# Performance work log

Hardware: AMD Instinct MI355X
Metric: run time of the kernel (lower is better)

## Reference

```python
import jax, jax.numpy as jnp
import numpy as np

HIDDEN = 4096
INTER = 11008
BATCH, SEQ = 2, 2048


def setup_inputs() -> dict:
    key = jax.random.key(0)
    ks = jax.random.split(key, 7)
    s_h = 1.0 / np.sqrt(HIDDEN)   # nn.Linear default init bound fan_in=HIDDEN
    s_i = 1.0 / np.sqrt(INTER)    # fan_in=INTER for down_proj
    return {
        "hidden_states": jax.random.normal(ks[0], (BATCH, SEQ, HIDDEN), dtype=jnp.float32),
        "w_gate": jax.random.uniform(ks[1], (INTER, HIDDEN), jnp.float32, -s_h, s_h),
        "b_gate": jax.random.uniform(ks[2], (INTER,), jnp.float32, -s_h, s_h),
        "w_up": jax.random.uniform(ks[3], (INTER, HIDDEN), jnp.float32, -s_h, s_h),
        "b_up": jax.random.uniform(ks[4], (INTER,), jnp.float32, -s_h, s_h),
        "w_down": jax.random.uniform(ks[5], (HIDDEN, INTER), jnp.float32, -s_i, s_i),
        "b_down": jax.random.uniform(ks[6], (HIDDEN,), jnp.float32, -s_i, s_i),
    }


def reference(hidden_states, w_gate, b_gate, w_up, b_up, w_down, b_down):
    # SwiGLU MLP: down( silu(gate(x)) * up(x) )
    gate = jax.nn.silu(jnp.einsum("bsh,ih->bsi", hidden_states, w_gate) + b_gate)
    up = jnp.einsum("bsh,ih->bsi", hidden_states, w_up) + b_up
    return jnp.einsum("bsi,hi->bsh", gate * up, w_down) + b_down
```

## Files before the change

### kernel.cpp

```cpp
#include <hip/hip_runtime.h>
#include <hip/hip_bf16.h>


#define M_TOK 4096
#define HID   4096
#define INT_  11008

typedef __attribute__((ext_vector_type(8))) short bf16x8;
typedef __attribute__((ext_vector_type(4))) float f32x4;

__device__ __forceinline__ unsigned short f2bf(float f) {
    union { float f; unsigned int u; } a; a.f = f;
    unsigned int u = a.u;
    u += 0x7fff + ((u >> 16) & 1);
    return (unsigned short)(u >> 16);
}

__device__ __forceinline__ float bf2f(unsigned short h) {
    union { unsigned int u; float f; } a; a.u = ((unsigned int)h) << 16;
    return a.f;
}

__global__ void cvt_f32_bf16(const float* __restrict__ in, unsigned short* __restrict__ out, int n4) {
    int stride = gridDim.x * blockDim.x;
    for (int i = blockIdx.x * blockDim.x + threadIdx.x; i < n4; i += stride) {
        float4 v = ((const float4*)in)[i];
        ushort4 o;
        o.x = f2bf(v.x); o.y = f2bf(v.y); o.z = f2bf(v.z); o.w = f2bf(v.w);
        ((ushort4*)out)[i] = o;
    }
}

#define GLL(gsrc, ldst) \
    __builtin_amdgcn_global_load_lds( \
        (__attribute__((address_space(1))) void*)(gsrc), \
        (__attribute__((address_space(3))) void*)(ldst), 16, 0, 0)

template<int EPI>
__global__ __launch_bounds__(512, 2)
void gemm256(const unsigned short* __restrict__ A,
             const unsigned short* __restrict__ B,
             const float* __restrict__ bias,
             const unsigned short* __restrict__ gbuf,
             void* __restrict__ Cv,
             int M, int N, int K) {
    __shared__ unsigned short lds[2 * 32768];

    const int tid  = threadIdx.x;
    const int lane = tid & 63;
    const int w    = tid >> 6;
    const int wm   = w >> 2;
    const int wn   = w & 3;

    const int ntn = N >> 8;
    const int chunk = gridDim.x >> 3;
    const int sw = (blockIdx.x & 7) * chunk + (blockIdx.x >> 3);
    const int bm = sw / ntn, bn = sw % ntn;

    const unsigned short* Ag = A + (size_t)(bm * 256) * K;
    const unsigned short* Bg = B + (size_t)(bn * 256) * K;

    int offA[2][2], offB[2][2];
#pragma unroll
    for (int h = 0; h < 2; ++h)
#pragma unroll
        for (int i = 0; i < 2; ++i) {
            int sig = i * 512 + tid;
            int r   = sig >> 3;
            int s   = (sig & 7) ^ (r & 7);
            int grow = ((r >> 6) * 2 + h) * 64 + (r & 63);
            int gcol = ((r >> 5) * 2 + h) * 32 + (r & 31);
            offA[h][i] = grow * K + s * 8;
            offB[h][i] = gcol * K + s * 8;
        }

    const int rl = lane & 15;
    const int kg = lane >> 4;
    const int x  = rl & 7;
    const int aRow = (wm * 64 + rl) * 64;
    const int bRow = 16384 + (wn * 32 + rl) * 64;
    int slt[2];
#pragma unroll
    for (int ks = 0; ks < 2; ++ks) slt[ks] = ((ks * 4 + kg) ^ x) * 8;

    f32x4 acc[2][2][8];
#pragma unroll
    for (int qm = 0; qm < 2; ++qm)
#pragma unroll
        for (int qn = 0; qn < 2; ++qn)
#pragma unroll
            for (int f = 0; f < 8; ++f)
                acc[qm][qn][f] = (f32x4){0.f, 0.f, 0.f, 0.f};

    const int NT = K >> 6;

#define STAGE_A(H, DST, SRC) \
    GLL((SRC) + offA[H][0], (DST) + (H) * 8192 + tid * 8); \
    GLL((SRC) + offA[H][1], (DST) + (H) * 8192 + 4096 + tid * 8)
#define STAGE_B(H, DST, SRC) \
    GLL((SRC) + offB[H][0], (DST) + 16384 + (H) * 8192 + tid * 8); \
    GLL((SRC) + offB[H][1], (DST) + 16384 + (H) * 8192 + 4096 + tid * 8)

#define RD_A(BUF, QM, DST) \
    { _Pragma("unroll") for (int ks = 0; ks < 2; ++ks) \
      _Pragma("unroll") for (int fm = 0; fm < 4; ++fm) \
        DST[ks * 4 + fm] = *(const bf16x8*)((BUF) + (QM) * 8192 + aRow + fm * 1024 + slt[ks]); }
#define RD_B(BUF, QN, DST) \
    { _Pragma("unroll") for (int ks = 0; ks < 2; ++ks) \
      _Pragma("unroll") for (int fn = 0; fn < 2; ++fn) \
        DST[ks * 2 + fn] = *(const bf16x8*)((BUF) + (QN) * 8192 + bRow + fn * 1024 + slt[ks]); }
#define Q16(QM, QN, AF, BF) \
    { _Pragma("unroll") for (int ks = 0; ks < 2; ++ks) \
      _Pragma("unroll") for (int fm = 0; fm < 4; ++fm) \
      _Pragma("unroll") for (int fn = 0; fn < 2; ++fn) \
        acc[QM][QN][fm * 2 + fn] = __builtin_amdgcn_mfma_f32_16x16x32_bf16( \
            AF[ks * 4 + fm], BF[ks * 2 + fn], acc[QM][QN][fm * 2 + fn], 0, 0, 0); }
#define VMC(n) asm volatile("s_waitcnt vmcnt(" #n ")" ::: "memory")
#define BARR __builtin_amdgcn_s_barrier()
#define PIN  __builtin_amdgcn_sched_barrier(0)

    bf16x8 A0f[8], A1f[8], B0f[4], B1f[4];

    STAGE_A(0, lds, Ag); STAGE_B(0, lds, Bg); STAGE_B(1, lds, Bg); STAGE_A(1, lds, Ag);
    VMC(2);
    BARR; PIN;

    for (int t = 0; t < NT; ++t) {
        const unsigned short* bc = lds + (t & 1) * 32768;
        unsigned short* sb = lds + ((t + 1) & 1) * 32768;
        const int ts = (t + 1 < NT) ? (t + 1) : (NT - 1);
        const unsigned short* sAt = Ag + (size_t)ts * 64;
        const unsigned short* sBt = Bg + (size_t)ts * 64;

        RD_A(bc, 0, A0f);
        RD_B(bc, 0, B0f);
        STAGE_A(0, sb, sAt);
        Q16(0, 0, A0f, B0f);
        RD_B(bc, 1, B1f);
        STAGE_B(0, sb, sBt);
        Q16(0, 1, A0f, B1f);
        STAGE_B(1, sb, sBt);
        VMC(6);
        BARR; PIN;

        RD_A(bc, 1, A1f);
        STAGE_A(1, sb, sAt);
        Q16(1, 1, A1f, B1f);
        Q16(1, 0, A1f, B0f);
        VMC(2);
        BARR; PIN;
    }
#undef RD_A
#undef RD_B
#undef Q16
#undef VMC
#undef BARR
#undef PIN
#undef STAGE_A
#undef STAGE_B

    const int rbase = bm * 256 + wm * 128 + (lane >> 4) * 4;
    const int cbase = bn * 256 + wn * 64 + (lane & 15);
#pragma unroll
    for (int qm = 0; qm < 2; ++qm)
#pragma unroll
        for (int qn = 0; qn < 2; ++qn)
#pragma unroll
            for (int fn = 0; fn < 2; ++fn) {
                const int col = cbase + qn * 32 + fn * 16;
                const float bv = bias[col];
#pragma unroll
                for (int fm = 0; fm < 4; ++fm) {
                    const int rb = rbase + qm * 64 + fm * 16;
#pragma unroll
                    for (int j = 0; j < 4; ++j) {
                        const size_t idx = (size_t)(rb + j) * (size_t)N + col;
                        float v = acc[qm][qn][fm * 2 + fn][j] + bv;
                        if (EPI == 0) {
                            ((unsigned short*)Cv)[idx] = f2bf(v);
                        } else if (EPI == 1) {
                            float g = bf2f(gbuf[idx]);
                            float s = g / (1.f + __expf(-g));
                            ((unsigned short*)Cv)[idx] = f2bf(s * v);
                        } else {
                            ((float*)Cv)[idx] = v;
                        }
                    }
                }
            }
}

extern "C" void kernel_launch(void* const* d_in, const int* in_sizes, int n_in,
                              void* d_out, int out_size, void* d_ws, size_t ws_size,
                              hipStream_t stream) {
    const float* x  = (const float*)d_in[0];
    const float* wg = (const float*)d_in[1];
    const float* bg = (const float*)d_in[2];
    const float* wu = (const float*)d_in[3];
    const float* bu = (const float*)d_in[4];
    const float* wd = (const float*)d_in[5];
    const float* bd = (const float*)d_in[6];

    const size_t NX = (size_t)M_TOK * HID;
    const size_t NW = (size_t)INT_ * HID;

    unsigned short* ws = (unsigned short*)d_ws;
    unsigned short* Xb = ws;
    unsigned short* S1 = Xb + NX;
    unsigned short* S2 = S1 + NW;
    unsigned short* S3 = S2 + NW;

    dim3 blk512(512);
    dim3 blk256(256);
    const int CG = 2048;

    cvt_f32_bf16<<<CG, blk256, 0, stream>>>(x,  Xb, (int)(NX / 4));
    cvt_f32_bf16<<<CG, blk256, 0, stream>>>(wg, S1, (int)(NW / 4));
    gemm256<0><<<dim3(16 * 43), blk512, 0, stream>>>(Xb, S1, bg, (const unsigned short*)nullptr,
                                                     (void*)S2, M_TOK, INT_, HID);
    cvt_f32_bf16<<<CG, blk256, 0, stream>>>(wu, S3, (int)(NW / 4));
    gemm256<1><<<dim3(16 * 43), blk512, 0, stream>>>(Xb, S3, bu, S2,
                                                     (void*)S1, M_TOK, INT_, HID);
    cvt_f32_bf16<<<CG, blk256, 0, stream>>>(wd, S2, (int)(NW / 4));
    gemm256<2><<<dim3(16 * 16), blk512, 0, stream>>>(S1, S2, bd, (const unsigned short*)nullptr,
                                                     d_out, M_TOK, HID, INT_);
}
```

Measured before the change: 1.079 ms.

## Fuse gate and up projections into one dual-weight GEMM with SwiGLU epilogue

Replaces the separate gate and up GEMMs with a single kernel that computes 256x128 tiles of both projections, sharing each staged A tile between the two weight matrices. The SiLU-times-up product is applied in the epilogue, so the intermediate gate tensor is never written to and re-read from memory. The grid doubles to cover the narrower N tiles. In exchange, each A tile is now loaded once per 128 columns instead of once per 256, and the tile shape changes.

Measured after the change: 1.013 ms. 1.06x faster.

```diff
diff --git a/kernel.cpp b/kernel.cpp
--- a/kernel.cpp
+++ b/kernel.cpp
@@ -36,13 +36,161 @@
         (__attribute__((address_space(1))) void*)(gsrc), \
         (__attribute__((address_space(3))) void*)(ldst), 16, 0, 0)
 
-template<int EPI>
+#define VMC(n) asm volatile("s_waitcnt vmcnt(" #n ")" ::: "memory")
+#define BARR __builtin_amdgcn_s_barrier()
+#define PIN  __builtin_amdgcn_sched_barrier(0)
+
 __global__ __launch_bounds__(512, 2)
-void gemm256(const unsigned short* __restrict__ A,
+void gemm_gu(const unsigned short* __restrict__ A,
+             const unsigned short* __restrict__ Wg,
+             const unsigned short* __restrict__ Wu,
+             const float* __restrict__ bg,
+             const float* __restrict__ bu,
+             unsigned short* __restrict__ T,
+             int M, int NI, int K) {
+    __shared__ unsigned short lds[2 * 32768];
+
+    const int tid  = threadIdx.x;
+    const int lane = tid & 63;
+    const int w    = tid >> 6;
+    const int wm   = w >> 2;
+    const int wn   = w & 3;
+
+    const int ntn = NI >> 7;
+    const int chunk = gridDim.x >> 3;
+    const int sw = (blockIdx.x & 7) * chunk + (blockIdx.x >> 3);
+    const int bm = sw / ntn, bn = sw % ntn;
+
+    const unsigned short* Ag  = A  + (size_t)(bm * 256) * K;
+    const unsigned short* Bgg = Wg + (size_t)(bn * 128) * K;
+    const unsigned short* Bug = Wu + (size_t)(bn * 128) * K;
+
+    int offA[2][2], offBW[2];
+#pragma unroll
+    for (int i = 0; i < 2; ++i) {
+        int sig = i * 512 + tid;
+        int r   = sig >> 3;
+        int s   = (sig & 7) ^ (r & 7);
+#pragma unroll
+        for (int h = 0; h < 2; ++h) {
+            int grow = ((r >> 6) * 2 + h) * 64 + (r & 63);
+            offA[h][i] = grow * K + s * 8;
+        }
+        offBW[i] = r * K + s * 8;
+    }
+
+    const int rl = lane & 15;
+    const int kg = lane >> 4;
+    const int x  = rl & 7;
+    const int aRow  = (wm * 64 + rl) * 64;
+    const int bGoff = 16384 + (wn * 32 + rl) * 64;
+    const int bUoff = 24576 + (wn * 32 + rl) * 64;
+    int slt[2];
+#pragma unroll
+    for (int ks = 0; ks < 2; ++ks) slt[ks] = ((ks * 4 + kg) ^ x) * 8;
+
+    f32x4 accg[2][8], accu[2][8];
+#pragma unroll
+    for (int q = 0; q < 2; ++q)
+#pragma unroll
+        for (int f = 0; f < 8; ++f) {
+            accg[q][f] = (f32x4){0.f, 0.f, 0.f, 0.f};
+            accu[q][f] = (f32x4){0.f, 0.f, 0.f, 0.f};
+        }
+
+    const int NT = K >> 6;
+
+#define STAGE_A(H, DST, SRC) \
+    GLL((SRC) + offA[H][0], (DST) + (H) * 8192 + tid * 8); \
+    GLL((SRC) + offA[H][1], (DST) + (H) * 8192 + 4096 + tid * 8)
+#define STAGE_W(BASE, DST, SRC) \
+    GLL((SRC) + offBW[0], (DST) + (BASE) + tid * 8); \
+    GLL((SRC) + offBW[1], (DST) + (BASE) + 4096 + tid * 8)
+
+#define RD_A(BUF, QM, DST) \
+    { _Pragma("unroll") for (int ks = 0; ks < 2; ++ks) \
+      _Pragma("unroll") for (int fm = 0; fm < 4; ++fm) \
+        DST[ks * 4 + fm] = *(const bf16x8*)((BUF) + (QM) * 8192 + aRow + fm * 1024 + slt[ks]); }
+#define RD_W(BUF, ROFF, DST) \
+    { _Pragma("unroll") for (int ks = 0; ks < 2; ++ks) \
+      _Pragma("unroll") for (int fn = 0; fn < 2; ++fn) \
+        DST[ks * 2 + fn] = *(const bf16x8*)((BUF) + (ROFF) + fn * 1024 + slt[ks]); }
+#define Q16(ACC, QM, AF, BF) \
+    { _Pragma("unroll") for (int ks = 0; ks < 2; ++ks) \
+      _Pragma("unroll") for (int fm = 0; fm < 4; ++fm) \
+      _Pragma("unroll") for (int fn = 0; fn < 2; ++fn) \
+        ACC[QM][fm * 2 + fn] = __builtin_amdgcn_mfma_f32_16x16x32_bf16( \
+            AF[ks * 4 + fm], BF[ks * 2 + fn], ACC[QM][fm * 2 + fn], 0, 0, 0); }
+
+    bf16x8 A0f[8], A1f[8], Bgf[4], Buf_[4];
+
+    STAGE_A(0, lds, Ag);
+    STAGE_W(16384, lds, Bgg);
+    STAGE_W(24576, lds, Bug);
+    STAGE_A(1, lds, Ag);
+    VMC(2);
+    BARR; PIN;
+
+    for (int t = 0; t < NT; ++t) {
+        const unsigned short* bc = lds + (t & 1) * 32768;
+        unsigned short* sb = lds + ((t + 1) & 1) * 32768;
+        const int ts = (t + 1 < NT) ? (t + 1) : (NT - 1);
+        const unsigned short* sA = Ag + (size_t)ts * 64;
+        const unsigned short* sG = Bgg + (size_t)ts * 64;
+        const unsigned short* sU = Bug + (size_t)ts * 64;
+
+        RD_A(bc, 0, A0f);
+        RD_W(bc, bGoff, Bgf);
+        STAGE_A(0, sb, sA);
+        Q16(accg, 0, A0f, Bgf);
+        RD_W(bc, bUoff, Buf_);
+        STAGE_W(16384, sb, sG);
+        Q16(accu, 0, A0f, Buf_);
+        STAGE_W(24576, sb, sU);
+        VMC(6);
+        BARR; PIN;
+
+        RD_A(bc, 1, A1f);
+        STAGE_A(1, sb, sA);
+        Q16(accg, 1, A1f, Bgf);
+        Q16(accu, 1, A1f, Buf_);
+        VMC(2);
+        BARR; PIN;
+    }
+#undef RD_A
+#undef RD_W
+#undef Q16
+#undef STAGE_A
+#undef STAGE_W
+
+    const int rbase = bm * 256 + wm * 128 + (lane >> 4) * 4;
+    const int cbase = bn * 128 + wn * 32 + (lane & 15);
+#pragma unroll
+    for (int qm = 0; qm < 2; ++qm)
+#pragma unroll
+        for (int fn = 0; fn < 2; ++fn) {
+            const int col = cbase + fn * 16;
+            const float bgv = bg[col];
+            const float buv = bu[col];
+#pragma unroll
+            for (int fm = 0; fm < 4; ++fm) {
+                const int rb = rbase + qm * 64 + fm * 16;
+#pragma unroll
+                for (int j = 0; j < 4; ++j) {
+                    float g = accg[qm][fm * 2 + fn][j] + bgv;
+                    float u = accu[qm][fm * 2 + fn][j] + buv;
+                    float s = g / (1.f + __expf(-g)) * u;
+                    T[(size_t)(rb + j) * (size_t)INT_ + col] = f2bf(s);
+                }
+            }
+        }
+}
+
+__global__ __launch_bounds__(512, 2)
+void gemm_dn(const unsigned short* __restrict__ A,
              const unsigned short* __restrict__ B,
              const float* __restrict__ bias,
-             const unsigned short* __restrict__ gbuf,
-             void* __restrict__ Cv,
+             float* __restrict__ C,
              int M, int N, int K) {
     __shared__ unsigned short lds[2 * 32768];
 
@@ -100,7 +248,6 @@
 #define STAGE_B(H, DST, SRC) \
     GLL((SRC) + offB[H][0], (DST) + 16384 + (H) * 8192 + tid * 8); \
     GLL((SRC) + offB[H][1], (DST) + 16384 + (H) * 8192 + 4096 + tid * 8)
-
 #define RD_A(BUF, QM, DST) \
     { _Pragma("unroll") for (int ks = 0; ks < 2; ++ks) \
       _Pragma("unroll") for (int fm = 0; fm < 4; ++fm) \
@@ -115,9 +262,6 @@
       _Pragma("unroll") for (int fn = 0; fn < 2; ++fn) \
         acc[QM][QN][fm * 2 + fn] = __builtin_amdgcn_mfma_f32_16x16x32_bf16( \
             AF[ks * 4 + fm], BF[ks * 2 + fn], acc[QM][QN][fm * 2 + fn], 0, 0, 0); }
-#define VMC(n) asm volatile("s_waitcnt vmcnt(" #n ")" ::: "memory")
-#define BARR __builtin_amdgcn_s_barrier()
-#define PIN  __builtin_amdgcn_sched_barrier(0)
 
     bf16x8 A0f[8], A1f[8], B0f[4], B1f[4];
 
@@ -153,9 +297,6 @@
 #undef RD_A
 #undef RD_B
 #undef Q16
-#undef VMC
-#undef BARR
-#undef PIN
 #undef STAGE_A
 #undef STAGE_B
 
@@ -173,19 +314,8 @@
                 for (int fm = 0; fm < 4; ++fm) {
                     const int rb = rbase + qm * 64 + fm * 16;
 #pragma unroll
-                    for (int j = 0; j < 4; ++j) {
-                        const size_t idx = (size_t)(rb + j) * (size_t)N + col;
-                        float v = acc[qm][qn][fm * 2 + fn][j] + bv;
-                        if (EPI == 0) {
-                            ((unsigned short*)Cv)[idx] = f2bf(v);
-                        } else if (EPI == 1) {
-                            float g = bf2f(gbuf[idx]);
-                            float s = g / (1.f + __expf(-g));
-                            ((unsigned short*)Cv)[idx] = f2bf(s * v);
-                        } else {
-                            ((float*)Cv)[idx] = v;
-                        }
-                    }
+                    for (int j = 0; j < 4; ++j)
+                        C[(size_t)(rb + j) * (size_t)N + col] = acc[qm][qn][fm * 2 + fn][j] + bv;
                 }
             }
 }
@@ -216,12 +346,10 @@
 
     cvt_f32_bf16<<<CG, blk256, 0, stream>>>(x,  Xb, (int)(NX / 4));
     cvt_f32_bf16<<<CG, blk256, 0, stream>>>(wg, S1, (int)(NW / 4));
-    gemm256<0><<<dim3(16 * 43), blk512, 0, stream>>>(Xb, S1, bg, (const unsigned short*)nullptr,
-                                                     (void*)S2, M_TOK, INT_, HID);
-    cvt_f32_bf16<<<CG, blk256, 0, stream>>>(wu, S3, (int)(NW / 4));
-    gemm256<1><<<dim3(16 * 43), blk512, 0, stream>>>(Xb, S3, bu, S2,
-                                                     (void*)S1, M_TOK, INT_, HID);
-    cvt_f32_bf16<<<CG, blk256, 0, stream>>>(wd, S2, (int)(NW / 4));
-    gemm256<2><<<dim3(16 * 16), blk512, 0, stream>>>(S1, S2, bd, (const unsigned short*)nullptr,
-                                                     d_out, M_TOK, HID, INT_);
-}
+    cvt_f32_bf16<<<CG, blk256, 0, stream>>>(wu, S2, (int)(NW / 4));
+    gemm_gu<<<dim3(16 * 86), blk512, 0, stream>>>(Xb, S1, S2, bg, bu, S3,
+                                                  M_TOK, INT_, HID);
+    cvt_f32_bf16<<<CG, blk256, 0, stream>>>(wd, S1, (int)(NW / 4));
+    gemm_dn<<<dim3(16 * 16), blk512, 0, stream>>>(S3, S1, bd, (float*)d_out,
+                                                  M_TOK, HID, INT_);
+}
```
